# Performance work log

Measured on AMD Instinct MI355X. Metric: run time of the kernel, lower is better.

## Reference

```python
import jax, jax.numpy as jnp
import numpy as np

B, N, DIM = 4, 8192, 512
HEADS, DIM_HEAD = 8, 64
INNER = HEADS * DIM_HEAD


def setup_inputs() -> dict:
    key = jax.random.key(0)
    k1, k2, k3 = jax.random.split(key, 3)
    feats = jax.random.normal(k1, (B, N, DIM), dtype=jnp.float32)
    mask = jnp.ones((B, N), dtype=bool)
    w_qkv = jax.random.normal(k2, (DIM, INNER * 3), dtype=jnp.float32) * 0.02
    w_out = jax.random.normal(k3, (INNER, DIM), dtype=jnp.float32) * 0.02
    b_out = jnp.zeros((DIM,), dtype=jnp.float32)
    return {"feats": feats, "mask": mask, "w_qkv": w_qkv, "w_out": w_out, "b_out": b_out}


def reference(feats, mask, w_qkv, w_out, b_out):
    b, n, _ = feats.shape
    h, d = HEADS, DIM_HEAD
    scale = d ** -0.5

    qkv = feats @ w_qkv                               # [b, n, 3*inner]
    q, k, v = jnp.split(qkv, 3, axis=-1)
    # 'b n (h d) -> b h n d'
    to_heads = lambda t: t.reshape(b, n, h, d).transpose(0, 2, 1, 3)
    q, k, v = to_heads(q), to_heads(k), to_heads(v)

    m = mask[:, None, :, None]                        # 'b n -> b 1 n 1'
    neg = jnp.finfo(k.dtype).max
    k = jnp.where(m, k, -neg)
    v = jnp.where(m, v, 0.0)

    q = jax.nn.softmax(q, axis=-1) * scale            # softmax over d
    k = jax.nn.softmax(k, axis=-2)                    # softmax over n

    context = jnp.einsum('bhnd,bhne->bhde', k, v)     # [b, h, d, d]
    out = jnp.einsum('bhde,bhnd->bhne', context, q)   # [b, h, n, d]
    out = out.transpose(0, 2, 1, 3).reshape(b, n, h * d)
    return out @ w_out + b_out
```

## Files before the change

### kernel.cpp

```cpp
#include <hip/hip_runtime.h>

#define BB 4
#define NN 8192
#define DIM 512
#define HEADS 8
#define INNER 512
#define QKVW 1536
#define BN_ROWS 32768
#define KC 16

typedef __attribute__((ext_vector_type(8))) short bf16x8;
typedef __attribute__((ext_vector_type(8))) ushort u16x8;
typedef __attribute__((ext_vector_type(4))) float f32x4;

__device__ __forceinline__ ushort f2b(float x) {
  unsigned u = __float_as_uint(x);
  u = (u + 0x7FFFu + ((u >> 16) & 1u)) >> 16;
  return (ushort)u;
}
__device__ __forceinline__ float b2f(ushort u) {
  return __uint_as_float((unsigned)u << 16);
}

__device__ __forceinline__ void gload16(const ushort* src, ushort* lds) {
  __builtin_amdgcn_global_load_lds(
      (const __attribute__((address_space(1))) void*)src,
      (__attribute__((address_space(3))) void*)lds, 16, 0, 0);
}

#define BAR() __builtin_amdgcn_s_barrier()
#define LGKM0() do { asm volatile("s_waitcnt lgkmcnt(0)" ::: "memory"); \
                     __builtin_amdgcn_sched_barrier(0); } while (0)
#define VMC4() asm volatile("s_waitcnt vmcnt(4)" ::: "memory")
#define VMC0() asm volatile("s_waitcnt vmcnt(0)" ::: "memory")

template<int MODE>
__global__ __launch_bounds__(512, 2) void gemm_nt_bf16(
    const ushort* __restrict__ A, const ushort* __restrict__ BT,
    void* __restrict__ Cv, const float* __restrict__ bias,
    ushort* __restrict__ T1, ushort* __restrict__ T2,
    int K, int lda, int ldb, int ldc, long sA, long sB, long sC)
{
  const int gx = gridDim.x;
  const int nwg = gx * gridDim.y;
  const int hid = blockIdx.y * gx + blockIdx.x;
  const int lid = (hid & 7) * (nwg >> 3) + (hid >> 3);
  const int bx = lid % gx, by = lid / gx;

  const int bz = blockIdx.z;
  const long row0 = (long)by * 256;
  const int col0 = bx * 256;
  const ushort* Ag = A + (long)bz * sA + row0 * (long)lda;
  const ushort* Bg = BT + (long)bz * sB + (long)col0 * ldb;
  ushort* Cb = (ushort*)Cv + (long)bz * sC;
  float*  Cf = (float*)Cv + (long)bz * sC;

  __shared__ alignas(16) ushort smem[65536];
  auto Asb = [&](int buf) { return smem + buf * 16384; };
  auto Bsb = [&](int buf) { return smem + 32768 + buf * 16384; };

  const int tid = threadIdx.x;
  const int lane = tid & 63, wv = tid >> 6;
  const int wm = wv >> 2, wn = wv & 3;
  const int l15 = lane & 15, l4 = lane >> 4;

  auto stageA = [&](int buf, int half, int kt) {
#pragma unroll
    for (int i = 0; i < 2; i++) {
      int ci = i * 512 + tid;
      int r = ci >> 3, p = ci & 7;
      gload16(Ag + (long)(half * 128 + r) * lda + kt * 64 + ((p ^ (r & 7)) << 3),
              Asb(buf) + half * 8192 + ci * 8);
    }
  };
  auto stageB = [&](int buf, int half, int kt) {
#pragma unroll
    for (int i = 0; i < 2; i++) {
      int ci = i * 512 + tid;
      int r = ci >> 3, p = ci & 7;
      gload16(Bg + (long)(half * 128 + r) * ldb + kt * 64 + ((p ^ (r & 7)) << 3),
              Bsb(buf) + half * 8192 + ci * 8);
    }
  };
  auto rdA = [&](int buf, int mi, int s) {
    int rr = wm * 128 + mi * 16 + l15;
    return *(const bf16x8*)(Asb(buf) + rr * 64 + (((4 * s + l4) ^ (rr & 7)) << 3));
  };
  auto rdB = [&](int buf, int ni, int s) {
    int rr = wn * 64 + ni * 16 + l15;
    return *(const bf16x8*)(Bsb(buf) + rr * 64 + (((4 * s + l4) ^ (rr & 7)) << 3));
  };

  bf16x8 af[4][2], bfr[4][2];
  f32x4 acc[8][4] = {};

  auto mfmaQ = [&](int mh, int nh) {
    __builtin_amdgcn_s_setprio(1);
#pragma unroll
    for (int mi = 0; mi < 4; mi++)
#pragma unroll
      for (int ni = 0; ni < 2; ni++)
#pragma unroll
        for (int s = 0; s < 2; s++)
          acc[mh * 4 + mi][nh * 2 + ni] = __builtin_amdgcn_mfma_f32_16x16x32_bf16(
              af[mi][s], bfr[nh * 2 + ni][s], acc[mh * 4 + mi][nh * 2 + ni], 0, 0, 0);
    __builtin_amdgcn_s_setprio(0);
  };

  stageA(0, 0, 0); stageA(0, 1, 0); stageB(0, 0, 0); stageB(0, 1, 0);
  stageB(1, 0, 1); stageB(1, 1, 1);
  VMC4(); BAR();

  const int NT = K >> 6;
  for (int j = 0; j < (NT >> 1); j++) {
    const int Te = 2 * j, To = 2 * j + 1;
    const bool more = (Te + 2) < NT;
#pragma unroll
    for (int mi = 0; mi < 4; mi++) { af[mi][0] = rdA(0, mi, 0); af[mi][1] = rdA(0, mi, 1); }
#pragma unroll
    for (int ni = 0; ni < 2; ni++) { bfr[ni][0] = rdB(0, ni, 0); bfr[ni][1] = rdB(0, ni, 1); }
    stageA(1, 0, To);
    BAR(); LGKM0(); mfmaQ(0, 0); BAR();
#pragma unroll
    for (int ni = 2; ni < 4; ni++) { bfr[ni][0] = rdB(0, ni, 0); bfr[ni][1] = rdB(0, ni, 1); }
    stageA(1, 1, To);
    BAR(); LGKM0(); mfmaQ(0, 1); BAR();
#pragma unroll
    for (int mi = 0; mi < 4; mi++) { af[mi][0] = rdA(0, mi + 4, 0); af[mi][1] = rdA(0, mi + 4, 1); }
    if (more) stageB(0, 0, Te + 2);
    BAR(); LGKM0(); mfmaQ(1, 1); BAR();
    if (more) stageB(0, 1, Te + 2);
    BAR(); mfmaQ(1, 0);
    if (more) VMC4(); else VMC0();
    BAR();
#pragma unroll
    for (int mi = 0; mi < 4; mi++) { af[mi][0] = rdA(1, mi, 0); af[mi][1] = rdA(1, mi, 1); }
#pragma unroll
    for (int ni = 0; ni < 2; ni++) { bfr[ni][0] = rdB(1, ni, 0); bfr[ni][1] = rdB(1, ni, 1); }
    if (more) stageA(0, 0, Te + 2);
    BAR(); LGKM0(); mfmaQ(0, 0); BAR();
#pragma unroll
    for (int ni = 2; ni < 4; ni++) { bfr[ni][0] = rdB(1, ni, 0); bfr[ni][1] = rdB(1, ni, 1); }
    if (more) stageA(0, 1, Te + 2);
    BAR(); LGKM0(); mfmaQ(0, 1); BAR();
#pragma unroll
    for (int mi = 0; mi < 4; mi++) { af[mi][0] = rdA(1, mi + 4, 0); af[mi][1] = rdA(1, mi + 4, 1); }
    if (To + 2 < NT) stageB(1, 0, To + 2);
    BAR(); LGKM0(); mfmaQ(1, 1); BAR();
    if (To + 2 < NT) stageB(1, 1, To + 2);
    BAR(); mfmaQ(1, 0); VMC4(); BAR();
  }

  const int colg0 = col0 + wn * 64;
  const long rowg0 = row0 + wm * 128;

  if constexpr (MODE == 0) {
#pragma unroll
    for (int mi = 0; mi < 8; mi++)
#pragma unroll
      for (int ni = 0; ni < 4; ni++) {
        int cc = colg0 + ni * 16 + l15;
        float bv = bias[cc];
#pragma unroll
        for (int e = 0; e < 4; e++) {
          long rr = rowg0 + mi * 16 + l4 * 4 + e;
          Cf[rr * (long)ldc + cc] = acc[mi][ni][e] + bv;
        }
      }
  } else {
    const int sect = bx >> 1;
    if (sect == 0) {
#pragma unroll
      for (int mi = 0; mi < 8; mi++) {
        float ex[4][4];
        float s[4] = {0.f, 0.f, 0.f, 0.f};
#pragma unroll
        for (int ni = 0; ni < 4; ni++)
#pragma unroll
          for (int e = 0; e < 4; e++) {
            ex[ni][e] = __expf(acc[mi][ni][e]);
            s[e] += ex[ni][e];
          }
#pragma unroll
        for (int e = 0; e < 4; e++) {
          float t = s[e];
#pragma unroll
          for (int off = 1; off <= 8; off <<= 1) t += __shfl_xor(t, off);
          s[e] = 0.125f / t;
        }
#pragma unroll
        for (int ni = 0; ni < 4; ni++) {
          int cc = colg0 + ni * 16 + l15;
#pragma unroll
          for (int e = 0; e < 4; e++) {
            long rr = rowg0 + mi * 16 + l4 * 4 + e;
            Cb[rr * (long)ldc + cc] = f2b(ex[ni][e] * s[e]);
          }
        }
      }
    } else {
#pragma unroll
      for (int mi = 0; mi < 8; mi++)
#pragma unroll
        for (int ni = 0; ni < 4; ni++) {
          int c_loc = wn * 64 + ni * 16 + l15;
          int rbase = wm * 128 + mi * 16 + l4 * 4;
          ushort4 pk;
          float v0 = acc[mi][ni][0], v1 = acc[mi][ni][1];
          float v2 = acc[mi][ni][2], v3 = acc[mi][ni][3];
          if (sect == 1) { v0 = __expf(v0); v1 = __expf(v1); v2 = __expf(v2); v3 = __expf(v3); }
          pk.x = f2b(v0); pk.y = f2b(v1); pk.z = f2b(v2); pk.w = f2b(v3);
          int chunk = (rbase >> 3) ^ (c_loc & 31);
          *(ushort4*)&smem[c_loc * 256 + (chunk << 3) + (rbase & 7)] = pk;
        }
      __syncthreads();
      ushort* Tdst = (sect == 1) ? T1 : T2;
      const int c = tid >> 1, hf = tid & 1;
      const int dg0 = col0 - sect * 512;
      const int bb = (int)(row0 >> 13);
      const long nb = row0 & 8191;
      ushort* dst = Tdst + ((long)bb * 512 + dg0 + c) * 8192 + nb + hf * 128;
#pragma unroll
      for (int jj = 0; jj < 16; jj++) {
        int phys = (hf * 16 + jj) ^ (c & 31);
        *(u16x8*)(dst + jj * 8) = *(const u16x8*)&smem[c * 256 + phys * 8];
      }
    }
  }
}

__global__ __launch_bounds__(256) void cvt_f32_bf16(const float* __restrict__ in,
                                                    ushort* __restrict__ out)
{
  long i = ((long)blockIdx.x * 256 + threadIdx.x) * 8;
  float4 a = *(const float4*)(in + i);
  float4 b = *(const float4*)(in + i + 4);
  u16x8 o;
  o[0] = f2b(a.x); o[1] = f2b(a.y); o[2] = f2b(a.z); o[3] = f2b(a.w);
  o[4] = f2b(b.x); o[5] = f2b(b.y); o[6] = f2b(b.z); o[7] = f2b(b.w);
  *(u16x8*)(out + i) = o;
}

__global__ __launch_bounds__(256) void cvt_wqkvT(const float* __restrict__ in,
                                                 ushort* __restrict__ out)
{
  int idx = blockIdx.x * 256 + threadIdx.x;
  int n = idx >> 9, k = idx & 511;
  out[idx] = f2b(in[(long)k * QKVW + n]);
}

__global__ __launch_bounds__(256) void ctx_mfma_kernel(
    const ushort* __restrict__ ekT, const ushort* __restrict__ vT,
    float* __restrict__ ctx_p, float* __restrict__ den_p)
{
  const int bh = blockIdx.y, kc = blockIdx.x;
  const int b = bh >> 3, h = bh & 7;
  const long base = ((long)b * 512 + h * 64) * 8192 + kc * (NN / KC);
  const ushort* Ae = ekT + base;
  const ushort* Vv = vT + base;

  __shared__ alignas(16) ushort Asm[64 * 64];
  __shared__ alignas(16) ushort Bsm[64 * 64];

  const int tid = threadIdx.x, lane = tid & 63, wv = tid >> 6;
  const int wr = wv >> 1, wc = wv & 1;
  const int l15 = lane & 15, l4 = lane >> 4;

  f32x4 acc[2][2] = {};
  float dacc[2] = {0.f, 0.f};

  for (int k0 = 0; k0 < NN / KC; k0 += 64) {
    __syncthreads();
#pragma unroll
    for (int i = 0; i < 2; i++) {
      int ci = i * 256 + tid;
      int r = ci >> 3, p = ci & 7;
      gload16(Ae + (long)r * 8192 + k0 + ((p ^ (r & 7)) << 3), &Asm[ci * 8]);
    }
#pragma unroll
    for (int i = 0; i < 2; i++) {
      int ci = i * 256 + tid;
      int r = ci >> 3, p = ci & 7;
      gload16(Vv + (long)r * 8192 + k0 + ((p ^ (r & 7)) << 3), &Bsm[ci * 8]);
    }
    __syncthreads();

    bf16x8 af[2][2], bfr[2][2];
#pragma unroll
    for (int mi = 0; mi < 2; mi++)
#pragma unroll
      for (int s = 0; s < 2; s++) {
        int r = wr * 32 + mi * 16 + l15;
        af[mi][s] = *(const bf16x8*)&Asm[r * 64 + (((s * 4 + l4) ^ (r & 7)) << 3)];
      }
#pragma unroll
    for (int ni = 0; ni < 2; ni++)
#pragma unroll
      for (int s = 0; s < 2; s++) {
        int r = wc * 32 + ni * 16 + l15;
        bfr[ni][s] = *(const bf16x8*)&Bsm[r * 64 + (((s * 4 + l4) ^ (r & 7)) << 3)];
      }
#pragma unroll
    for (int mi = 0; mi < 2; mi++)
#pragma unroll
      for (int ni = 0; ni < 2; ni++)
#pragma unroll
        for (int s = 0; s < 2; s++)
          acc[mi][ni] = __builtin_amdgcn_mfma_f32_16x16x32_bf16(
              af[mi][s], bfr[ni][s], acc[mi][ni], 0, 0, 0);
    if (wc == 0) {
#pragma unroll
      for (int mi = 0; mi < 2; mi++)
#pragma unroll
        for (int s = 0; s < 2; s++) {
          float t = 0.f;
#pragma unroll
          for (int e = 0; e < 8; e++) t += b2f((ushort)af[mi][s][e]);
          dacc[mi] += t;
        }
    }
  }

  if (wc == 0) {
#pragma unroll
    for (int mi = 0; mi < 2; mi++) {
      float t = dacc[mi];
      t += __shfl_xor(t, 16);
      t += __shfl_xor(t, 32);
      if (l4 == 0)
        den_p[(bh * KC + kc) * 64 + wr * 32 + mi * 16 + l15] = t;
    }
  }

  float* cp = ctx_p + ((long)bh * KC + kc) * 4096;
#pragma unroll
  for (int mi = 0; mi < 2; mi++)
#pragma unroll
    for (int ni = 0; ni < 2; ni++)
#pragma unroll
      for (int e = 0; e < 4; e++)
        cp[(wr * 32 + mi * 16 + l4 * 4 + e) * 64 + wc * 32 + ni * 16 + l15] = acc[mi][ni][e];
}

__global__ __launch_bounds__(256) void ctx_reduce_kernel(
    const float* __restrict__ ctx_p, const float* __restrict__ den_p,
    float* __restrict__ ctx)
{
  const int bh = blockIdx.x;
  const int tid = threadIdx.x;
  __shared__ float den[64];
  if (tid < 64) {
    float s = 0.f;
    for (int c = 0; c < KC; c++) s += den_p[(bh * KC + c) * 64 + tid];
    den[tid] = s;
  }
  __syncthreads();
  for (int i = tid; i < 4096; i += 256) {
    int d = i >> 6;
    float s = 0.f;
    for (int c = 0; c < KC; c++) s += ctx_p[(long)(bh * KC + c) * 4096 + i];
    ctx[(long)bh * 4096 + i] = s / den[d];
  }
}

__global__ __launch_bounds__(256) void w2_kernel(
    const float* __restrict__ ctx, const float* __restrict__ w_out,
    ushort* __restrict__ W2T)
{
  const int bh = blockIdx.y, jc = blockIdx.x;
  const int b = bh >> 3, h = bh & 7;
  __shared__ float cs[64][65];
  for (int i = threadIdx.x; i < 4096; i += 256)
    cs[i >> 6][i & 63] = ctx[(long)bh * 4096 + i];
  __syncthreads();
  const int tx = threadIdx.x & 31, ty = threadIdx.x >> 5;
  float acc[8][4] = {};
  for (int e = 0; e < 64; e++) {
    float4 w = *(const float4*)&w_out[(long)(h * 64 + e) * DIM + jc * 128 + tx * 4];
#pragma unroll
    for (int i = 0; i < 8; i++) {
      float a = cs[ty * 8 + i][e];
      acc[i][0] = fmaf(a, w.x, acc[i][0]);
      acc[i][1] = fmaf(a, w.y, acc[i][1]);
      acc[i][2] = fmaf(a, w.z, acc[i][2]);
      acc[i][3] = fmaf(a, w.w, acc[i][3]);
    }
  }
#pragma unroll
  for (int i = 0; i < 8; i++)
#pragma unroll
    for (int q = 0; q < 4; q++) {
      int j = jc * 128 + tx * 4 + q;
      int k = h * 64 + ty * 8 + i;
      W2T[((long)b * DIM + j) * DIM + k] = f2b(acc[i][q]);
    }
}

extern "C" void kernel_launch(void* const* d_in, const int* in_sizes, int n_in,
                              void* d_out, int out_size, void* d_ws, size_t ws_size,
                              hipStream_t stream)
{
  const float* feats = (const float*)d_in[0];
  const float* w_qkv = (const float*)d_in[2];
  const float* w_out = (const float*)d_in[3];
  const float* b_out = (const float*)d_in[4];
  float* out = (float*)d_out;

  ushort* qsm = (ushort*)d_ws;
  ushort* ekT = qsm + (long)BN_ROWS * DIM;
  ushort* vT  = ekT + (long)BB * DIM * NN;
  ushort* feb = vT + (long)BB * DIM * NN;
  ushort* wqT = feb + (long)BN_ROWS * DIM;
  ushort* w2t = wqT + (long)QKVW * DIM;
  float* ctx_p  = (float*)(w2t + (long)BB * DIM * DIM);
  float* den_p  = ctx_p + (long)32 * KC * 4096;
  float* ctx    = den_p + 32 * KC * 64;

  cvt_f32_bf16<<<dim3((BN_ROWS * DIM) / (256 * 8)), 256, 0, stream>>>(feats, feb);
  cvt_wqkvT<<<dim3((QKVW * DIM) / 256), 256, 0, stream>>>(w_qkv, wqT);

  gemm_nt_bf16<1><<<dim3(QKVW / 256, BN_ROWS / 256, 1), 512, 0, stream>>>(
      feb, wqT, qsm, nullptr, ekT, vT, DIM, DIM, DIM, 512, 0, 0, 0);

  ctx_mfma_kernel<<<dim3(KC, 32), 256, 0, stream>>>(ekT, vT, ctx_p, den_p);

  ctx_reduce_kernel<<<dim3(32), 256, 0, stream>>>(ctx_p, den_p, ctx);

  w2_kernel<<<dim3(4, 32), 256, 0, stream>>>(ctx, w_out, w2t);

  gemm_nt_bf16<0><<<dim3(DIM / 256, NN / 256, BB), 512, 0, stream>>>(
      qsm, w2t, out, b_out, nullptr, nullptr, DIM, DIM, DIM, DIM,
      (long)NN * DIM, (long)DIM * DIM, (long)NN * DIM);
}
```

Baseline: 160.0 us.

## Fuse fp32-to-bf16 feature conversion into QKV GEMM A-tile loading

Drops the separate kernel that converted feats to bf16. The QKV GEMM now reads fp32 A tiles into registers, converts them to bf16 and writes them swizzled into LDS. This removes a full write and re-read of the bf16 copy of feats, plus one launch. The cost is twice the global bytes per A tile, since each of the 6 column blocks re-reads fp32 A, along with more registers and synchronous LDS writes that may limit overlap or occupancy.

```diff
diff --git a/kernel.cpp b/kernel.cpp
--- a/kernel.cpp
+++ b/kernel.cpp
@@ -36,7 +36,7 @@
 
 template<int MODE>
 __global__ __launch_bounds__(512, 2) void gemm_nt_bf16(
-    const ushort* __restrict__ A, const ushort* __restrict__ BT,
+    const void* __restrict__ Av, const ushort* __restrict__ BT,
     void* __restrict__ Cv, const float* __restrict__ bias,
     ushort* __restrict__ T1, ushort* __restrict__ T2,
     int K, int lda, int ldb, int ldc, long sA, long sB, long sC)
@@ -50,7 +50,8 @@
   const int bz = blockIdx.z;
   const long row0 = (long)by * 256;
   const int col0 = bx * 256;
-  const ushort* Ag = A + (long)bz * sA + row0 * (long)lda;
+  const ushort* Ag = (MODE == 0) ? ((const ushort*)Av + (long)bz * sA + row0 * (long)lda) : nullptr;
+  const float*  Af = (MODE == 1) ? ((const float*)Av + row0 * (long)lda) : nullptr;
   const ushort* Bg = BT + (long)bz * sB + (long)col0 * ldb;
   ushort* Cb = (ushort*)Cv + (long)bz * sC;
   float*  Cf = (float*)Cv + (long)bz * sC;
@@ -82,6 +83,22 @@
               Bsb(buf) + half * 8192 + ci * 8);
     }
   };
+  float4 ar0[4], ar1[4];
+#define ALOAD(H, kt) do { \
+  _Pragma("unroll") for (int i = 0; i < 2; i++) { \
+    int ci = i * 512 + tid; int r = ci >> 3, p = ci & 7; \
+    const float* sp = Af + (long)((H) * 128 + r) * lda + (kt) * 64 + ((p ^ (r & 7)) << 3); \
+    ar##H[2 * i]     = *(const float4*)sp; \
+    ar##H[2 * i + 1] = *(const float4*)(sp + 4); } } while (0)
+#define AWRITE(H, buf) do { \
+  _Pragma("unroll") for (int i = 0; i < 2; i++) { \
+    int ci = i * 512 + tid; \
+    float4 a0 = ar##H[2 * i], a1 = ar##H[2 * i + 1]; \
+    u16x8 pk; \
+    pk[0] = f2b(a0.x); pk[1] = f2b(a0.y); pk[2] = f2b(a0.z); pk[3] = f2b(a0.w); \
+    pk[4] = f2b(a1.x); pk[5] = f2b(a1.y); pk[6] = f2b(a1.z); pk[7] = f2b(a1.w); \
+    *(u16x8*)(Asb(buf) + (H) * 8192 + ci * 8) = pk; } } while (0)
+
   auto rdA = [&](int buf, int mi, int s) {
     int rr = wm * 128 + mi * 16 + l15;
     return *(const bf16x8*)(Asb(buf) + rr * 64 + (((4 * s + l4) ^ (rr & 7)) << 3));
@@ -107,9 +124,20 @@
     __builtin_amdgcn_s_setprio(0);
   };
 
-  stageA(0, 0, 0); stageA(0, 1, 0); stageB(0, 0, 0); stageB(0, 1, 0);
-  stageB(1, 0, 1); stageB(1, 1, 1);
-  VMC4(); BAR();
+  if constexpr (MODE == 0) {
+    stageA(0, 0, 0); stageA(0, 1, 0);
+    stageB(0, 0, 0); stageB(0, 1, 0);
+    stageB(1, 0, 1); stageB(1, 1, 1);
+    VMC4();
+  } else {
+    ALOAD(0, 0); ALOAD(1, 0);
+    stageB(0, 0, 0); stageB(0, 1, 0);
+    stageB(1, 0, 1); stageB(1, 1, 1);
+    VMC4();
+    AWRITE(0, 0); AWRITE(1, 0);
+    LGKM0();
+  }
+  BAR();
 
   const int NT = K >> 6;
   for (int j = 0; j < (NT >> 1); j++) {
@@ -119,11 +147,11 @@
     for (int mi = 0; mi < 4; mi++) { af[mi][0] = rdA(0, mi, 0); af[mi][1] = rdA(0, mi, 1); }
 #pragma unroll
     for (int ni = 0; ni < 2; ni++) { bfr[ni][0] = rdB(0, ni, 0); bfr[ni][1] = rdB(0, ni, 1); }
-    stageA(1, 0, To);
+    if constexpr (MODE == 0) stageA(1, 0, To); else ALOAD(0, To);
     BAR(); LGKM0(); mfmaQ(0, 0); BAR();
 #pragma unroll
     for (int ni = 2; ni < 4; ni++) { bfr[ni][0] = rdB(0, ni, 0); bfr[ni][1] = rdB(0, ni, 1); }
-    stageA(1, 1, To);
+    if constexpr (MODE == 0) stageA(1, 1, To); else ALOAD(1, To);
     BAR(); LGKM0(); mfmaQ(0, 1); BAR();
 #pragma unroll
     for (int mi = 0; mi < 4; mi++) { af[mi][0] = rdA(0, mi + 4, 0); af[mi][1] = rdA(0, mi + 4, 1); }
@@ -132,24 +160,32 @@
     if (more) stageB(0, 1, Te + 2);
     BAR(); mfmaQ(1, 0);
     if (more) VMC4(); else VMC0();
+    if constexpr (MODE == 1) { AWRITE(0, 1); AWRITE(1, 1); LGKM0(); }
     BAR();
 #pragma unroll
     for (int mi = 0; mi < 4; mi++) { af[mi][0] = rdA(1, mi, 0); af[mi][1] = rdA(1, mi, 1); }
 #pragma unroll
     for (int ni = 0; ni < 2; ni++) { bfr[ni][0] = rdB(1, ni, 0); bfr[ni][1] = rdB(1, ni, 1); }
-    if (more) stageA(0, 0, Te + 2);
+    if (more) { if constexpr (MODE == 0) stageA(0, 0, Te + 2); else ALOAD(0, Te + 2); }
     BAR(); LGKM0(); mfmaQ(0, 0); BAR();
 #pragma unroll
     for (int ni = 2; ni < 4; ni++) { bfr[ni][0] = rdB(1, ni, 0); bfr[ni][1] = rdB(1, ni, 1); }
-    if (more) stageA(0, 1, Te + 2);
+    if (more) { if constexpr (MODE == 0) stageA(0, 1, Te + 2); else ALOAD(1, Te + 2); }
     BAR(); LGKM0(); mfmaQ(0, 1); BAR();
 #pragma unroll
     for (int mi = 0; mi < 4; mi++) { af[mi][0] = rdA(1, mi + 4, 0); af[mi][1] = rdA(1, mi + 4, 1); }
     if (To + 2 < NT) stageB(1, 0, To + 2);
     BAR(); LGKM0(); mfmaQ(1, 1); BAR();
     if (To + 2 < NT) stageB(1, 1, To + 2);
-    BAR(); mfmaQ(1, 0); VMC4(); BAR();
-  }
+    BAR(); mfmaQ(1, 0);
+    if (more) {
+      VMC4();
+      if constexpr (MODE == 1) { AWRITE(0, 0); AWRITE(1, 0); LGKM0(); }
+    }
+    BAR();
+  }
+#undef ALOAD
+#undef AWRITE
 
   const int colg0 = col0 + wn * 64;
   const long rowg0 = row0 + wm * 128;
@@ -229,18 +265,6 @@
   }
 }
 
-__global__ __launch_bounds__(256) void cvt_f32_bf16(const float* __restrict__ in,
-                                                    ushort* __restrict__ out)
-{
-  long i = ((long)blockIdx.x * 256 + threadIdx.x) * 8;
-  float4 a = *(const float4*)(in + i);
-  float4 b = *(const float4*)(in + i + 4);
-  u16x8 o;
-  o[0] = f2b(a.x); o[1] = f2b(a.y); o[2] = f2b(a.z); o[3] = f2b(a.w);
-  o[4] = f2b(b.x); o[5] = f2b(b.y); o[6] = f2b(b.z); o[7] = f2b(b.w);
-  *(u16x8*)(out + i) = o;
-}
-
 __global__ __launch_bounds__(256) void cvt_wqkvT(const float* __restrict__ in,
                                                  ushort* __restrict__ out)
 {
@@ -409,18 +433,16 @@
   ushort* qsm = (ushort*)d_ws;
   ushort* ekT = qsm + (long)BN_ROWS * DIM;
   ushort* vT  = ekT + (long)BB * DIM * NN;
-  ushort* feb = vT + (long)BB * DIM * NN;
-  ushort* wqT = feb + (long)BN_ROWS * DIM;
+  ushort* wqT = vT + (long)BB * DIM * NN;
   ushort* w2t = wqT + (long)QKVW * DIM;
   float* ctx_p  = (float*)(w2t + (long)BB * DIM * DIM);
   float* den_p  = ctx_p + (long)32 * KC * 4096;
   float* ctx    = den_p + 32 * KC * 64;
 
-  cvt_f32_bf16<<<dim3((BN_ROWS * DIM) / (256 * 8)), 256, 0, stream>>>(feats, feb);
   cvt_wqkvT<<<dim3((QKVW * DIM) / 256), 256, 0, stream>>>(w_qkv, wqT);
 
   gemm_nt_bf16<1><<<dim3(QKVW / 256, BN_ROWS / 256, 1), 512, 0, stream>>>(
-      feb, wqT, qsm, nullptr, ekT, vT, DIM, DIM, DIM, 512, 0, 0, 0);
+      feats, wqT, qsm, nullptr, ekT, vT, DIM, DIM, DIM, 512, 0, 0, 0);
 
   ctx_mfma_kernel<<<dim3(KC, 32), 256, 0, stream>>>(ekT, vT, ctx_p, den_p);
 
```

Result: slower. 184.3 us (+15.2%).

## Write transposed K/V directly from registers and fuse ctx reduce with W2 kernel

Applied to the files above, without the earlier changes.

The QKV GEMM epilogue for the exp(K) and V sections no longer stages tiles through swizzled LDS for coalesced transposed stores. Each lane now writes its 4-element bf16 vectors straight to the transposed global layout, which removes a __syncthreads and the LDS round trip but produces scattered 8-byte stores. Separately, the context reduction and the context×w_out product are merged into one kernel. This drops a launch and the ctx global buffer, but cuts parallelism from 128 blocks to 32 blocks that each loop over four column chunks.

```diff
diff --git a/kernel.cpp b/kernel.cpp
--- a/kernel.cpp
+++ b/kernel.cpp
@@ -199,32 +199,23 @@
         }
       }
     } else {
+      ushort* Tdst = (sect == 1) ? T1 : T2;
+      const int bb = (int)(row0 >> 13);
+      const long nb = row0 & 8191;
+      const int dg0 = col0 - sect * 512 + wn * 64;
 #pragma unroll
       for (int mi = 0; mi < 8; mi++)
 #pragma unroll
         for (int ni = 0; ni < 4; ni++) {
-          int c_loc = wn * 64 + ni * 16 + l15;
-          int rbase = wm * 128 + mi * 16 + l4 * 4;
-          ushort4 pk;
+          int d = dg0 + ni * 16 + l15;
+          long n = nb + wm * 128 + mi * 16 + l4 * 4;
           float v0 = acc[mi][ni][0], v1 = acc[mi][ni][1];
           float v2 = acc[mi][ni][2], v3 = acc[mi][ni][3];
           if (sect == 1) { v0 = __expf(v0); v1 = __expf(v1); v2 = __expf(v2); v3 = __expf(v3); }
+          ushort4 pk;
           pk.x = f2b(v0); pk.y = f2b(v1); pk.z = f2b(v2); pk.w = f2b(v3);
-          int chunk = (rbase >> 3) ^ (c_loc & 31);
-          *(ushort4*)&smem[c_loc * 256 + (chunk << 3) + (rbase & 7)] = pk;
+          *(ushort4*)&Tdst[((long)bb * 512 + d) * 8192 + n] = pk;
         }
-      __syncthreads();
-      ushort* Tdst = (sect == 1) ? T1 : T2;
-      const int c = tid >> 1, hf = tid & 1;
-      const int dg0 = col0 - sect * 512;
-      const int bb = (int)(row0 >> 13);
-      const long nb = row0 & 8191;
-      ushort* dst = Tdst + ((long)bb * 512 + dg0 + c) * 8192 + nb + hf * 128;
-#pragma unroll
-      for (int jj = 0; jj < 16; jj++) {
-        int phys = (hf * 16 + jj) ^ (c & 31);
-        *(u16x8*)(dst + jj * 8) = *(const u16x8*)&smem[c * 256 + phys * 8];
-      }
     }
   }
 }
@@ -342,12 +333,14 @@
         cp[(wr * 32 + mi * 16 + l4 * 4 + e) * 64 + wc * 32 + ni * 16 + l15] = acc[mi][ni][e];
 }
 
-__global__ __launch_bounds__(256) void ctx_reduce_kernel(
+__global__ __launch_bounds__(256) void ctxw2_kernel(
     const float* __restrict__ ctx_p, const float* __restrict__ den_p,
-    float* __restrict__ ctx)
+    const float* __restrict__ w_out, ushort* __restrict__ W2T)
 {
   const int bh = blockIdx.x;
+  const int b = bh >> 3, h = bh & 7;
   const int tid = threadIdx.x;
+  __shared__ float cs[64][65];
   __shared__ float den[64];
   if (tid < 64) {
     float s = 0.f;
@@ -356,44 +349,34 @@
   }
   __syncthreads();
   for (int i = tid; i < 4096; i += 256) {
-    int d = i >> 6;
     float s = 0.f;
     for (int c = 0; c < KC; c++) s += ctx_p[(long)(bh * KC + c) * 4096 + i];
-    ctx[(long)bh * 4096 + i] = s / den[d];
-  }
-}
-
-__global__ __launch_bounds__(256) void w2_kernel(
-    const float* __restrict__ ctx, const float* __restrict__ w_out,
-    ushort* __restrict__ W2T)
-{
-  const int bh = blockIdx.y, jc = blockIdx.x;
-  const int b = bh >> 3, h = bh & 7;
-  __shared__ float cs[64][65];
-  for (int i = threadIdx.x; i < 4096; i += 256)
-    cs[i >> 6][i & 63] = ctx[(long)bh * 4096 + i];
+    cs[i >> 6][i & 63] = s / den[i >> 6];
+  }
   __syncthreads();
-  const int tx = threadIdx.x & 31, ty = threadIdx.x >> 5;
-  float acc[8][4] = {};
-  for (int e = 0; e < 64; e++) {
-    float4 w = *(const float4*)&w_out[(long)(h * 64 + e) * DIM + jc * 128 + tx * 4];
-#pragma unroll
-    for (int i = 0; i < 8; i++) {
-      float a = cs[ty * 8 + i][e];
-      acc[i][0] = fmaf(a, w.x, acc[i][0]);
-      acc[i][1] = fmaf(a, w.y, acc[i][1]);
-      acc[i][2] = fmaf(a, w.z, acc[i][2]);
-      acc[i][3] = fmaf(a, w.w, acc[i][3]);
-    }
-  }
-#pragma unroll
-  for (int i = 0; i < 8; i++)
-#pragma unroll
-    for (int q = 0; q < 4; q++) {
-      int j = jc * 128 + tx * 4 + q;
-      int k = h * 64 + ty * 8 + i;
-      W2T[((long)b * DIM + j) * DIM + k] = f2b(acc[i][q]);
-    }
+  const int tx = tid & 31, ty = tid >> 5;
+  for (int jc = 0; jc < 4; jc++) {
+    float acc[8][4] = {};
+    for (int e = 0; e < 64; e++) {
+      float4 w = *(const float4*)&w_out[(long)(h * 64 + e) * DIM + jc * 128 + tx * 4];
+#pragma unroll
+      for (int i = 0; i < 8; i++) {
+        float a = cs[ty * 8 + i][e];
+        acc[i][0] = fmaf(a, w.x, acc[i][0]);
+        acc[i][1] = fmaf(a, w.y, acc[i][1]);
+        acc[i][2] = fmaf(a, w.z, acc[i][2]);
+        acc[i][3] = fmaf(a, w.w, acc[i][3]);
+      }
+    }
+#pragma unroll
+    for (int i = 0; i < 8; i++)
+#pragma unroll
+      for (int q = 0; q < 4; q++) {
+        int jcol = jc * 128 + tx * 4 + q;
+        int k = h * 64 + ty * 8 + i;
+        W2T[((long)b * DIM + jcol) * DIM + k] = f2b(acc[i][q]);
+      }
+  }
 }
 
 extern "C" void kernel_launch(void* const* d_in, const int* in_sizes, int n_in,
@@ -414,7 +397,6 @@
   ushort* w2t = wqT + (long)QKVW * DIM;
   float* ctx_p  = (float*)(w2t + (long)BB * DIM * DIM);
   float* den_p  = ctx_p + (long)32 * KC * 4096;
-  float* ctx    = den_p + 32 * KC * 64;
 
   cvt_f32_bf16<<<dim3((BN_ROWS * DIM) / (256 * 8)), 256, 0, stream>>>(feats, feb);
   cvt_wqkvT<<<dim3((QKVW * DIM) / 256), 256, 0, stream>>>(w_qkv, wqT);
@@ -424,9 +406,7 @@
 
   ctx_mfma_kernel<<<dim3(KC, 32), 256, 0, stream>>>(ekT, vT, ctx_p, den_p);
 
-  ctx_reduce_kernel<<<dim3(32), 256, 0, stream>>>(ctx_p, den_p, ctx);
-
-  w2_kernel<<<dim3(4, 32), 256, 0, stream>>>(ctx, w_out, w2t);
+  ctxw2_kernel<<<dim3(32), 256, 0, stream>>>(ctx_p, den_p, w_out, w2t);
 
   gemm_nt_bf16<0><<<dim3(DIM / 256, NN / 256, BB), 512, 0, stream>>>(
       qsm, w2t, out, b_out, nullptr, nullptr, DIM, DIM, DIM, DIM,
```

Result: slower. 178.7 us (+11.7%).
